# Kernel tuning notes

Hardware: AMD Instinct MI355X
Metric: run time of the kernel (lower is better)

Reference implementation:

```python
import jax, jax.numpy as jnp
import numpy as np

B, C, H, W = 8, 10, 128, 128  # batch, hidden_dim, spatial
EPS = 1e-5


def conv1x1(x, w, b=None):
    # x: [b, i, h, w], w: [o, i] -> [b, o, h, w]
    y = jnp.einsum('oi,bihw->bohw', w, x)
    if b is not None:
        y = y + b[None, :, None, None]
    return y


def bn(x, gamma, beta):
    # training-mode batchnorm over (N, H, W), as InPlaceABNSync(activation='none')
    m = x.mean(axis=(0, 2, 3), keepdims=True)
    v = x.var(axis=(0, 2, 3), keepdims=True)
    xn = (x - m) * jax.lax.rsqrt(v + EPS)
    return xn * gamma[None, :, None, None] + beta[None, :, None, None]


def conv_gru(x, h, wg, bg, wc):
    # ConvGRU with 1x1 kernels: gates conv -> 2 channels (reset, update)
    gates = conv1x1(jnp.concatenate([x, h], axis=1), wg, bg)  # [b,2,h,w]
    reset = jax.nn.sigmoid(gates[:, 0:1])
    update = jax.nn.sigmoid(gates[:, 1:2])
    cand = jnp.tanh(conv1x1(jnp.concatenate([x, reset * h], axis=1), wc))
    return (1.0 - update) * h + update * cand


def setup_inputs() -> dict:
    key = jax.random.key(0)
    ks = jax.random.split(key, 16)
    rn = lambda k, shape, s=1.0: jax.random.normal(k, shape, dtype=jnp.float32) * s
    inp = {
        'f0': rn(ks[0], (B, C, H, W)),
        'f1': rn(ks[1], (B, C, H, W)),
        'h0': rn(ks[2], (B, C, H, W)),
        'h1': rn(ks[3], (B, C, H, W)),
        'h2': rn(ks[4], (B, C, H, W)),
        # Composition.comp_att: Conv2d(2C -> 1, bias=True) + Sigmoid
        'W_att': rn(ks[5], (1, 2 * C), 0.1),
        'b_att': jnp.zeros((1,), jnp.float32),
        # Composition.relation: Conv(2C->2C, no bias) BN ReLU Conv(2C->C, no bias) BN ReLU
        'W_r1': rn(ks[6], (2 * C, 2 * C), 0.1),
        'g_r1': jnp.ones((2 * C,), jnp.float32),
        'be_r1': jnp.zeros((2 * C,), jnp.float32),
        'W_r2': rn(ks[7], (C, 2 * C), 0.1),
        'g_r2': jnp.ones((C,), jnp.float32),
        'be_r2': jnp.zeros((C,), jnp.float32),
        # ConvGRU update[0]: gates Conv(2C->2, bias) ; candidate Conv(2C->C, no bias)
        'Wg0': rn(ks[8], (2, 2 * C), 0.1),
        'bg0': jnp.zeros((2,), jnp.float32),
        'Wc0': rn(ks[9], (C, 2 * C), 0.1),
        # ConvGRU update[1]
        'Wg1': rn(ks[10], (2, 2 * C), 0.1),
        'bg1': jnp.zeros((2,), jnp.float32),
        'Wc1': rn(ks[11], (C, 2 * C), 0.1),
    }
    return inp


def reference(f0, f1, h0, h1, h2,
              W_att, b_att, W_r1, g_r1, be_r1, W_r2, g_r2, be_r2,
              Wg0, bg0, Wc0, Wg1, bg1, Wc1):
    # node 0: update[0](h_node_list[0], f_node_list[0])
    node0 = conv_gru(h0, f0, Wg0, bg0, Wc0)
    # Composition over children h1, h2
    comp_att = jax.nn.sigmoid(conv1x1(jnp.concatenate([h1, h2], axis=1), W_att, b_att))  # [b,1,h,w]
    x = jnp.concatenate([f1, (h1 + h2) * comp_att], axis=1)  # [b,2C,h,w]
    x = jax.nn.relu(bn(conv1x1(x, W_r1), g_r1, be_r1))
    comp_full = jax.nn.relu(bn(conv1x1(x, W_r2), g_r2, be_r2))  # [b,C,h,w]
    # node 1: update[1](comp_full, f_node_list[1])
    node1 = conv_gru(comp_full, f1, Wg1, bg1, Wc1)
    return node0, node1, comp_att
```

## Files before the change

### kernel.cpp

```cpp
#include <hip/hip_runtime.h>
#include <math.h>

#define HW     16384
#define NPIX   131072
#define NPLANE 1310720
#define TPB    64
#define NBLK   512
#define BN_N   131072.0f
#define EPS_BN 1e-5f

typedef float v4 __attribute__((ext_vector_type(4)));

__device__ __forceinline__ float sigf(float x) { return 1.0f / (1.0f + __expf(-x)); }
__device__ __forceinline__ float tanh_fast(float x) {
    x = fminf(fmaxf(x, -15.0f), 15.0f);
    float e = __expf(2.0f * x);
    return (e - 1.0f) / (e + 1.0f);
}
__device__ __forceinline__ v4 sig4(v4 x) {
    v4 r; r.x = sigf(x.x); r.y = sigf(x.y); r.z = sigf(x.z); r.w = sigf(x.w); return r;
}
__device__ __forceinline__ v4 tanh4(v4 x) {
    v4 r; r.x = tanh_fast(x.x); r.y = tanh_fast(x.y); r.z = tanh_fast(x.z); r.w = tanh_fast(x.w); return r;
}
__device__ __forceinline__ v4 relu4(v4 x) {
    v4 r; r.x = fmaxf(x.x, 0.f); r.y = fmaxf(x.y, 0.f); r.z = fmaxf(x.z, 0.f); r.w = fmaxf(x.w, 0.f); return r;
}
__device__ __forceinline__ float hsum4(v4 a) { return (a.x + a.y) + (a.z + a.w); }
__device__ __forceinline__ float dot4(v4 a)  { return a.x * a.x + a.y * a.y + a.z * a.z + a.w * a.w; }
__device__ __forceinline__ float wred(float v) {
#pragma unroll
    for (int o = 32; o; o >>= 1) v += __shfl_down(v, o, 64);
    return v;
}
__device__ __forceinline__ v4 ld4(const float* p) { return *(const v4*)p; }
__device__ __forceinline__ void nt_st4(v4 v, float* p) {
    __builtin_nontemporal_store(v, (v4*)p);
}

__global__ __launch_bounds__(TPB, 1) void kernA(
    const float* __restrict__ f0, const float* __restrict__ f1,
    const float* __restrict__ h0, const float* __restrict__ h1, const float* __restrict__ h2,
    const float* __restrict__ W_att, const float* __restrict__ b_att,
    const float* __restrict__ W_r1,
    const float* __restrict__ Wg0, const float* __restrict__ bg0, const float* __restrict__ Wc0,
    float* __restrict__ node0, float* __restrict__ att_out, float* __restrict__ stats)
{
    __shared__ float sP[40];
    const int tid = threadIdx.x;
    const int g = blockIdx.x * TPB + tid;
    const int b = g >> 12, sp = (g & 4095) << 2;
    const int base = b * (10 * HW) + sp;

    v4 vh1[10], vh2[10], vf1[10], vf0[10], vh0[10];
#pragma unroll
    for (int c = 0; c < 10; c++) {
        vh1[c] = ld4(h1 + base + c * HW);
        vh2[c] = ld4(h2 + base + c * HW);
        vf1[c] = ld4(f1 + base + c * HW);
        vf0[c] = ld4(f0 + base + c * HW);
        vh0[c] = ld4(h0 + base + c * HW);
    }

    v4 z = b_att[0];
#pragma unroll
    for (int c = 0; c < 10; c++) z += W_att[c] * vh1[c] + W_att[10 + c] * vh2[c];
    const v4 att = sig4(z);
    nt_st4(att, att_out + 4 * g);

    v4 x[20];
#pragma unroll
    for (int c = 0; c < 10; c++) { x[c] = vf1[c]; x[10 + c] = (vh1[c] + vh2[c]) * att; }
#pragma unroll
    for (int o = 0; o < 20; o++) {
        v4 acc = 0.0f;
#pragma unroll
        for (int i = 0; i < 20; i++) acc += W_r1[o * 20 + i] * x[i];
        float s = wred(hsum4(acc));
        float q = wred(dot4(acc));
        if (tid == 0) { sP[o] = s; sP[20 + o] = q; }
    }

    v4 g0 = bg0[0], g1 = bg0[1];
#pragma unroll
    for (int i = 0; i < 10; i++) {
        g0 += Wg0[i] * vh0[i] + Wg0[10 + i] * vf0[i];
        g1 += Wg0[20 + i] * vh0[i] + Wg0[30 + i] * vf0[i];
    }
    const v4 r = sig4(g0), u = sig4(g1);
#pragma unroll
    for (int o = 0; o < 10; o++) {
        v4 acc = 0.0f;
#pragma unroll
        for (int i = 0; i < 10; i++)
            acc += Wc0[o * 20 + i] * vh0[i] + Wc0[o * 20 + 10 + i] * (r * vf0[i]);
        nt_st4((1.0f - u) * vf0[o] + u * tanh4(acc), node0 + base + o * HW);
    }

    __syncthreads();
    if (tid < 40) atomicAdd(&stats[tid], sP[tid]);
}

__global__ __launch_bounds__(TPB, 1) void kernC(
    const float* __restrict__ f1, const float* __restrict__ h1, const float* __restrict__ h2,
    const float* __restrict__ W_att, const float* __restrict__ b_att,
    const float* __restrict__ W_r1, const float* __restrict__ g_r1, const float* __restrict__ be_r1,
    const float* __restrict__ W_r2,
    float* __restrict__ stats, float* __restrict__ y2out)
{
    __shared__ float sP[20];
    const int tid = threadIdx.x;
    const int g = blockIdx.x * TPB + tid;
    const int b = g >> 12, sp = (g & 4095) << 2;
    const int base = b * (10 * HW) + sp;

    v4 vf1[10], vh1[10], vh2[10];
#pragma unroll
    for (int c = 0; c < 10; c++) {
        vh1[c] = ld4(h1 + base + c * HW);
        vh2[c] = ld4(h2 + base + c * HW);
        vf1[c] = ld4(f1 + base + c * HW);
    }

    v4 z = b_att[0];
#pragma unroll
    for (int c = 0; c < 10; c++) z += W_att[c] * vh1[c] + W_att[10 + c] * vh2[c];
    const v4 att = sig4(z);

    v4 x[20];
#pragma unroll
    for (int c = 0; c < 10; c++) { x[c] = vf1[c]; x[10 + c] = (vh1[c] + vh2[c]) * att; }

    v4 x2[20];
#pragma unroll
    for (int o = 0; o < 20; o++) {
        v4 acc = 0.0f;
#pragma unroll
        for (int i = 0; i < 20; i++) acc += W_r1[o * 20 + i] * x[i];
        const float mean = stats[o] * (1.0f / BN_N);
        const float var  = stats[20 + o] * (1.0f / BN_N) - mean * mean;
        const float a  = g_r1[o] * rsqrtf(var + EPS_BN);
        const float bb = be_r1[o] - mean * a;
        x2[o] = relu4(a * acc + bb);
    }

#pragma unroll
    for (int o = 0; o < 10; o++) {
        v4 acc = 0.0f;
#pragma unroll
        for (int i = 0; i < 20; i++) acc += W_r2[o * 20 + i] * x2[i];
        *(v4*)(y2out + base + o * HW) = acc;
        float s = wred(hsum4(acc));
        float q = wred(dot4(acc));
        if (tid == 0) { sP[o] = s; sP[10 + o] = q; }
    }
    __syncthreads();
    if (tid < 20) atomicAdd(&stats[40 + tid], sP[tid]);
}

__global__ __launch_bounds__(TPB, 1) void kernE(
    const float* __restrict__ f1, const float* __restrict__ y2in,
    const float* __restrict__ stats,
    const float* __restrict__ g_r2, const float* __restrict__ be_r2,
    const float* __restrict__ Wg1, const float* __restrict__ bg1, const float* __restrict__ Wc1,
    float* __restrict__ node1)
{
    const int tid = threadIdx.x;
    const int g = blockIdx.x * TPB + tid;
    const int b = g >> 12, sp = (g & 4095) << 2;
    const int base = b * (10 * HW) + sp;

    v4 vf1[10], vy2[10];
#pragma unroll
    for (int c = 0; c < 10; c++) {
        vf1[c] = ld4(f1 + base + c * HW);
        vy2[c] = ld4(y2in + base + c * HW);
    }

    v4 comp[10];
#pragma unroll
    for (int c = 0; c < 10; c++) {
        const float mean = stats[40 + c] * (1.0f / BN_N);
        const float var  = stats[50 + c] * (1.0f / BN_N) - mean * mean;
        const float a  = g_r2[c] * rsqrtf(var + EPS_BN);
        const float bb = be_r2[c] - mean * a;
        comp[c] = relu4(a * vy2[c] + bb);
    }

    v4 g0 = bg1[0], g1 = bg1[1];
#pragma unroll
    for (int i = 0; i < 10; i++) {
        g0 += Wg1[i] * comp[i] + Wg1[10 + i] * vf1[i];
        g1 += Wg1[20 + i] * comp[i] + Wg1[30 + i] * vf1[i];
    }
    const v4 r = sig4(g0), u = sig4(g1);
#pragma unroll
    for (int o = 0; o < 10; o++) {
        v4 acc = 0.0f;
#pragma unroll
        for (int i = 0; i < 10; i++)
            acc += Wc1[o * 20 + i] * comp[i] + Wc1[o * 20 + 10 + i] * (r * vf1[i]);
        nt_st4((1.0f - u) * vf1[o] + u * tanh4(acc), node1 + base + o * HW);
    }
}

extern "C" void kernel_launch(void* const* d_in, const int* in_sizes, int n_in,
                              void* d_out, int out_size, void* d_ws, size_t ws_size,
                              hipStream_t stream) {
    const float* f0    = (const float*)d_in[0];
    const float* f1    = (const float*)d_in[1];
    const float* h0    = (const float*)d_in[2];
    const float* h1    = (const float*)d_in[3];
    const float* h2    = (const float*)d_in[4];
    const float* W_att = (const float*)d_in[5];
    const float* b_att = (const float*)d_in[6];
    const float* W_r1  = (const float*)d_in[7];
    const float* g_r1  = (const float*)d_in[8];
    const float* be_r1 = (const float*)d_in[9];
    const float* W_r2  = (const float*)d_in[10];
    const float* g_r2  = (const float*)d_in[11];
    const float* be_r2 = (const float*)d_in[12];
    const float* Wg0   = (const float*)d_in[13];
    const float* bg0   = (const float*)d_in[14];
    const float* Wc0   = (const float*)d_in[15];
    const float* Wg1   = (const float*)d_in[16];
    const float* bg1   = (const float*)d_in[17];
    const float* Wc1   = (const float*)d_in[18];

    float* out   = (float*)d_out;
    float* node0 = out;
    float* node1 = out + NPLANE;
    float* attO  = out + 2 * NPLANE;

    float* stats = (float*)d_ws;
    float* y2    = stats + 64;

    hipMemsetAsync(stats, 0, 64 * sizeof(float), stream);

    dim3 grid(NBLK), blk(TPB);
    kernA<<<grid, blk, 0, stream>>>(f0, f1, h0, h1, h2, W_att, b_att, W_r1,
                                    Wg0, bg0, Wc0, node0, attO, stats);
    kernC<<<grid, blk, 0, stream>>>(f1, h1, h2, W_att, b_att, W_r1, g_r1, be_r1,
                                    W_r2, stats, y2);
    kernE<<<grid, blk, 0, stream>>>(f1, y2, stats, g_r2, be_r2, Wg1, bg1, Wc1,
                                    node1);
}
```

Baseline: 160.4 us.

## Fuse three kernels into one persistent kernel with device-wide barriers

Replaces the three launches and the memset with one kernel. It uses agent-scope atomic grid barriers to wait for the two BatchNorm statistics reductions, and block 0 zeroes the stats and counters in-kernel. Each thread keeps f1, the relation input and the second conv output in registers across phases. This avoids re-reading h1/h2/f1, recomputing attention, and writing then reading the y2 intermediate. In exchange it depends on all 512 blocks being co-resident, carries higher register pressure, and risks a race on repeated launches because the ctl[0] ready flag is never reset.

```diff
diff --git a/kernel.cpp b/kernel.cpp
--- a/kernel.cpp
+++ b/kernel.cpp
@@ -38,28 +38,51 @@
     __builtin_nontemporal_store(v, (v4*)p);
 }
 
-__global__ __launch_bounds__(TPB, 1) void kernA(
+__device__ __forceinline__ void gbar(int* ctr, int target) {
+    __threadfence();
+    __syncthreads();
+    if (threadIdx.x == 0)
+        __hip_atomic_fetch_add(ctr, 1, __ATOMIC_ACQ_REL, __HIP_MEMORY_SCOPE_AGENT);
+    while (__hip_atomic_load(ctr, __ATOMIC_ACQUIRE, __HIP_MEMORY_SCOPE_AGENT) < target)
+        __builtin_amdgcn_s_sleep(8);
+}
+
+__global__ __launch_bounds__(TPB, 1) void fused(
     const float* __restrict__ f0, const float* __restrict__ f1,
     const float* __restrict__ h0, const float* __restrict__ h1, const float* __restrict__ h2,
     const float* __restrict__ W_att, const float* __restrict__ b_att,
-    const float* __restrict__ W_r1,
+    const float* __restrict__ W_r1, const float* __restrict__ g_r1, const float* __restrict__ be_r1,
+    const float* __restrict__ W_r2, const float* __restrict__ g_r2, const float* __restrict__ be_r2,
     const float* __restrict__ Wg0, const float* __restrict__ bg0, const float* __restrict__ Wc0,
-    float* __restrict__ node0, float* __restrict__ att_out, float* __restrict__ stats)
+    const float* __restrict__ Wg1, const float* __restrict__ bg1, const float* __restrict__ Wc1,
+    float* __restrict__ node0, float* __restrict__ node1, float* __restrict__ att_out,
+    int* __restrict__ ctl, float* __restrict__ stats)
 {
     __shared__ float sP[40];
+    __shared__ float sB[64];
     const int tid = threadIdx.x;
+
+    if (blockIdx.x == 0) {
+        if (tid < 60) __hip_atomic_store(&stats[tid], 0.0f, __ATOMIC_RELAXED, __HIP_MEMORY_SCOPE_AGENT);
+        if (tid < 2)  __hip_atomic_store(&ctl[32 + 32 * tid], 0, __ATOMIC_RELAXED, __HIP_MEMORY_SCOPE_AGENT);
+        __threadfence();
+        __syncthreads();
+        if (tid == 0) __hip_atomic_store(&ctl[0], 1, __ATOMIC_RELEASE, __HIP_MEMORY_SCOPE_AGENT);
+    }
+
     const int g = blockIdx.x * TPB + tid;
     const int b = g >> 12, sp = (g & 4095) << 2;
     const int base = b * (10 * HW) + sp;
 
-    v4 vh1[10], vh2[10], vf1[10], vf0[10], vh0[10];
+    v4 vh1[10], vh2[10], vf0[10], vh0[10];
+    v4 x[20];
 #pragma unroll
     for (int c = 0; c < 10; c++) {
-        vh1[c] = ld4(h1 + base + c * HW);
-        vh2[c] = ld4(h2 + base + c * HW);
-        vf1[c] = ld4(f1 + base + c * HW);
-        vf0[c] = ld4(f0 + base + c * HW);
-        vh0[c] = ld4(h0 + base + c * HW);
+        vh1[c]  = ld4(h1 + base + c * HW);
+        vh2[c]  = ld4(h2 + base + c * HW);
+        x[c]    = ld4(f1 + base + c * HW);
+        vf0[c]  = ld4(f0 + base + c * HW);
+        vh0[c]  = ld4(h0 + base + c * HW);
     }
 
     v4 z = b_att[0];
@@ -67,10 +90,9 @@
     for (int c = 0; c < 10; c++) z += W_att[c] * vh1[c] + W_att[10 + c] * vh2[c];
     const v4 att = sig4(z);
     nt_st4(att, att_out + 4 * g);
-
-    v4 x[20];
-#pragma unroll
-    for (int c = 0; c < 10; c++) { x[c] = vf1[c]; x[10 + c] = (vh1[c] + vh2[c]) * att; }
+#pragma unroll
+    for (int c = 0; c < 10; c++) x[10 + c] = (vh1[c] + vh2[c]) * att;
+
 #pragma unroll
     for (int o = 0; o < 20; o++) {
         v4 acc = 0.0f;
@@ -81,126 +103,92 @@
         if (tid == 0) { sP[o] = s; sP[20 + o] = q; }
     }
 
-    v4 g0 = bg0[0], g1 = bg0[1];
-#pragma unroll
-    for (int i = 0; i < 10; i++) {
-        g0 += Wg0[i] * vh0[i] + Wg0[10 + i] * vf0[i];
-        g1 += Wg0[20 + i] * vh0[i] + Wg0[30 + i] * vf0[i];
-    }
-    const v4 r = sig4(g0), u = sig4(g1);
-#pragma unroll
-    for (int o = 0; o < 10; o++) {
-        v4 acc = 0.0f;
-#pragma unroll
-        for (int i = 0; i < 10; i++)
-            acc += Wc0[o * 20 + i] * vh0[i] + Wc0[o * 20 + 10 + i] * (r * vf0[i]);
-        nt_st4((1.0f - u) * vf0[o] + u * tanh4(acc), node0 + base + o * HW);
-    }
-
-    __syncthreads();
+    {
+        v4 g0 = bg0[0], g1 = bg0[1];
+#pragma unroll
+        for (int i = 0; i < 10; i++) {
+            g0 += Wg0[i] * vh0[i] + Wg0[10 + i] * vf0[i];
+            g1 += Wg0[20 + i] * vh0[i] + Wg0[30 + i] * vf0[i];
+        }
+        const v4 r = sig4(g0), u = sig4(g1);
+#pragma unroll
+        for (int o = 0; o < 10; o++) {
+            v4 acc = 0.0f;
+#pragma unroll
+            for (int i = 0; i < 10; i++)
+                acc += Wc0[o * 20 + i] * vh0[i] + Wc0[o * 20 + 10 + i] * (r * vf0[i]);
+            nt_st4((1.0f - u) * vf0[o] + u * tanh4(acc), node0 + base + o * HW);
+        }
+    }
+
+    __syncthreads();
+    while (__hip_atomic_load(&ctl[0], __ATOMIC_ACQUIRE, __HIP_MEMORY_SCOPE_AGENT) != 1)
+        __builtin_amdgcn_s_sleep(8);
     if (tid < 40) atomicAdd(&stats[tid], sP[tid]);
-}
-
-__global__ __launch_bounds__(TPB, 1) void kernC(
-    const float* __restrict__ f1, const float* __restrict__ h1, const float* __restrict__ h2,
-    const float* __restrict__ W_att, const float* __restrict__ b_att,
-    const float* __restrict__ W_r1, const float* __restrict__ g_r1, const float* __restrict__ be_r1,
-    const float* __restrict__ W_r2,
-    float* __restrict__ stats, float* __restrict__ y2out)
-{
-    __shared__ float sP[20];
-    const int tid = threadIdx.x;
-    const int g = blockIdx.x * TPB + tid;
-    const int b = g >> 12, sp = (g & 4095) << 2;
-    const int base = b * (10 * HW) + sp;
-
-    v4 vf1[10], vh1[10], vh2[10];
-#pragma unroll
-    for (int c = 0; c < 10; c++) {
-        vh1[c] = ld4(h1 + base + c * HW);
-        vh2[c] = ld4(h2 + base + c * HW);
-        vf1[c] = ld4(f1 + base + c * HW);
-    }
-
-    v4 z = b_att[0];
-#pragma unroll
-    for (int c = 0; c < 10; c++) z += W_att[c] * vh1[c] + W_att[10 + c] * vh2[c];
-    const v4 att = sig4(z);
-
-    v4 x[20];
-#pragma unroll
-    for (int c = 0; c < 10; c++) { x[c] = vf1[c]; x[10 + c] = (vh1[c] + vh2[c]) * att; }
-
-    v4 x2[20];
-#pragma unroll
-    for (int o = 0; o < 20; o++) {
-        v4 acc = 0.0f;
-#pragma unroll
-        for (int i = 0; i < 20; i++) acc += W_r1[o * 20 + i] * x[i];
-        const float mean = stats[o] * (1.0f / BN_N);
-        const float var  = stats[20 + o] * (1.0f / BN_N) - mean * mean;
-        const float a  = g_r1[o] * rsqrtf(var + EPS_BN);
-        const float bb = be_r1[o] - mean * a;
-        x2[o] = relu4(a * acc + bb);
-    }
-
-#pragma unroll
-    for (int o = 0; o < 10; o++) {
-        v4 acc = 0.0f;
-#pragma unroll
-        for (int i = 0; i < 20; i++) acc += W_r2[o * 20 + i] * x2[i];
-        *(v4*)(y2out + base + o * HW) = acc;
-        float s = wred(hsum4(acc));
-        float q = wred(dot4(acc));
-        if (tid == 0) { sP[o] = s; sP[10 + o] = q; }
+
+    gbar(&ctl[32], NBLK);
+
+    if (tid < 40) sB[tid] = __hip_atomic_load(&stats[tid], __ATOMIC_RELAXED, __HIP_MEMORY_SCOPE_AGENT);
+    __syncthreads();
+
+    v4 y2[10];
+    {
+        v4 x2[20];
+#pragma unroll
+        for (int o = 0; o < 20; o++) {
+            v4 acc = 0.0f;
+#pragma unroll
+            for (int i = 0; i < 20; i++) acc += W_r1[o * 20 + i] * x[i];
+            const float mean = sB[o] * (1.0f / BN_N);
+            const float var  = sB[20 + o] * (1.0f / BN_N) - mean * mean;
+            const float a  = g_r1[o] * rsqrtf(var + EPS_BN);
+            const float bb = be_r1[o] - mean * a;
+            x2[o] = relu4(a * acc + bb);
+        }
+#pragma unroll
+        for (int o = 0; o < 10; o++) {
+            v4 acc = 0.0f;
+#pragma unroll
+            for (int i = 0; i < 20; i++) acc += W_r2[o * 20 + i] * x2[i];
+            y2[o] = acc;
+            float s = wred(hsum4(acc));
+            float q = wred(dot4(acc));
+            if (tid == 0) { sP[o] = s; sP[10 + o] = q; }
+        }
     }
     __syncthreads();
     if (tid < 20) atomicAdd(&stats[40 + tid], sP[tid]);
-}
-
-__global__ __launch_bounds__(TPB, 1) void kernE(
-    const float* __restrict__ f1, const float* __restrict__ y2in,
-    const float* __restrict__ stats,
-    const float* __restrict__ g_r2, const float* __restrict__ be_r2,
-    const float* __restrict__ Wg1, const float* __restrict__ bg1, const float* __restrict__ Wc1,
-    float* __restrict__ node1)
-{
-    const int tid = threadIdx.x;
-    const int g = blockIdx.x * TPB + tid;
-    const int b = g >> 12, sp = (g & 4095) << 2;
-    const int base = b * (10 * HW) + sp;
-
-    v4 vf1[10], vy2[10];
-#pragma unroll
-    for (int c = 0; c < 10; c++) {
-        vf1[c] = ld4(f1 + base + c * HW);
-        vy2[c] = ld4(y2in + base + c * HW);
-    }
-
-    v4 comp[10];
-#pragma unroll
-    for (int c = 0; c < 10; c++) {
-        const float mean = stats[40 + c] * (1.0f / BN_N);
-        const float var  = stats[50 + c] * (1.0f / BN_N) - mean * mean;
-        const float a  = g_r2[c] * rsqrtf(var + EPS_BN);
-        const float bb = be_r2[c] - mean * a;
-        comp[c] = relu4(a * vy2[c] + bb);
-    }
-
-    v4 g0 = bg1[0], g1 = bg1[1];
-#pragma unroll
-    for (int i = 0; i < 10; i++) {
-        g0 += Wg1[i] * comp[i] + Wg1[10 + i] * vf1[i];
-        g1 += Wg1[20 + i] * comp[i] + Wg1[30 + i] * vf1[i];
-    }
-    const v4 r = sig4(g0), u = sig4(g1);
-#pragma unroll
-    for (int o = 0; o < 10; o++) {
-        v4 acc = 0.0f;
-#pragma unroll
-        for (int i = 0; i < 10; i++)
-            acc += Wc1[o * 20 + i] * comp[i] + Wc1[o * 20 + 10 + i] * (r * vf1[i]);
-        nt_st4((1.0f - u) * vf1[o] + u * tanh4(acc), node1 + base + o * HW);
+
+    gbar(&ctl[64], NBLK);
+
+    if (tid < 20) sB[tid] = __hip_atomic_load(&stats[40 + tid], __ATOMIC_RELAXED, __HIP_MEMORY_SCOPE_AGENT);
+    __syncthreads();
+
+    {
+        v4 comp[10];
+#pragma unroll
+        for (int c = 0; c < 10; c++) {
+            const float mean = sB[c] * (1.0f / BN_N);
+            const float var  = sB[10 + c] * (1.0f / BN_N) - mean * mean;
+            const float a  = g_r2[c] * rsqrtf(var + EPS_BN);
+            const float bb = be_r2[c] - mean * a;
+            comp[c] = relu4(a * y2[c] + bb);
+        }
+        v4 g0 = bg1[0], g1 = bg1[1];
+#pragma unroll
+        for (int i = 0; i < 10; i++) {
+            g0 += Wg1[i] * comp[i] + Wg1[10 + i] * x[i];
+            g1 += Wg1[20 + i] * comp[i] + Wg1[30 + i] * x[i];
+        }
+        const v4 r = sig4(g0), u = sig4(g1);
+#pragma unroll
+        for (int o = 0; o < 10; o++) {
+            v4 acc = 0.0f;
+#pragma unroll
+            for (int i = 0; i < 10; i++)
+                acc += Wc1[o * 20 + i] * comp[i] + Wc1[o * 20 + 10 + i] * (r * x[i]);
+            nt_st4((1.0f - u) * x[o] + u * tanh4(acc), node1 + base + o * HW);
+        }
     }
 }
 
@@ -232,16 +220,12 @@
     float* node1 = out + NPLANE;
     float* attO  = out + 2 * NPLANE;
 
-    float* stats = (float*)d_ws;
-    float* y2    = stats + 64;
-
-    hipMemsetAsync(stats, 0, 64 * sizeof(float), stream);
-
-    dim3 grid(NBLK), blk(TPB);
-    kernA<<<grid, blk, 0, stream>>>(f0, f1, h0, h1, h2, W_att, b_att, W_r1,
-                                    Wg0, bg0, Wc0, node0, attO, stats);
-    kernC<<<grid, blk, 0, stream>>>(f1, h1, h2, W_att, b_att, W_r1, g_r1, be_r1,
-                                    W_r2, stats, y2);
-    kernE<<<grid, blk, 0, stream>>>(f1, y2, stats, g_r2, be_r2, Wg1, bg1, Wc1,
-                                    node1);
-}
+    int*   ctl   = (int*)d_ws;
+    float* stats = (float*)d_ws + 128;
+
+    fused<<<dim3(NBLK), dim3(TPB), 0, stream>>>(
+        f0, f1, h0, h1, h2, W_att, b_att,
+        W_r1, g_r1, be_r1, W_r2, g_r2, be_r2,
+        Wg0, bg0, Wc0, Wg1, bg1, Wc1,
+        node0, node1, attO, ctl, stats);
+}
```

Measured after the change: 217.8 us. 35.8% more time.
